# Optimization experiments

Measured on AMD Instinct MI355X. Metric: run time of the kernel, lower is better.

The kernel has to match this reference:

```python
import jax, jax.numpy as jnp
import numpy as np

B, P, C, O = 64, 24564, 81, 20
THRESHOLD = 0.5
NEG_POS_RATIO = 3
ALPHA = 1.0


def cxcy_to_xy(c):
    return jnp.concatenate([c[..., :2] - c[..., 2:] / 2, c[..., :2] + c[..., 2:] / 2], -1)


def xy_to_cxcy(x):
    return jnp.concatenate([(x[..., :2] + x[..., 2:]) / 2, x[..., 2:] - x[..., :2]], -1)


def cxcy_to_gcxgcy(c, p):
    # SSD box encoding with variances (10, 5)
    return jnp.concatenate([(c[..., :2] - p[..., :2]) / (p[..., 2:] / 10.0),
                            jnp.log(c[..., 2:] / p[..., 2:]) * 5.0], -1)


def jaccard(a, b):
    # a: [O,4] xy, b: [P,4] xy -> [O,P]
    lt = jnp.maximum(a[:, None, :2], b[None, :, :2])
    rb = jnp.minimum(a[:, None, 2:], b[None, :, 2:])
    wh = jnp.clip(rb - lt, 0.0)
    inter = wh[..., 0] * wh[..., 1]
    area_a = (a[:, 2] - a[:, 0]) * (a[:, 3] - a[:, 1])
    area_b = (b[:, 2] - b[:, 0]) * (b[:, 3] - b[:, 1])
    union = area_a[:, None] + area_b[None, :] - inter
    return inter / union


def smooth_l1(x):
    ax = jnp.abs(x)
    return jnp.where(ax < 1.0, 0.5 * ax * ax, ax - 0.5)


def setup_inputs() -> dict:
    key = jax.random.key(0)
    k1, k2, k3, k4, k5, k6, k7 = jax.random.split(key, 7)
    predicted_locs = jax.random.normal(k1, (B, P, 4), jnp.float32)
    predicted_scores = jax.random.normal(k2, (B, P, C), jnp.float32)
    # valid ground-truth boxes in boundary (xy) coords
    cxy = jax.random.uniform(k3, (B, O, 2), jnp.float32, 0.2, 0.8)
    wh = jax.random.uniform(k4, (B, O, 2), jnp.float32, 0.05, 0.3)
    boxes = jnp.concatenate([cxy - wh / 2, cxy + wh / 2], -1)
    labels = jax.random.randint(k5, (B, O), 1, C).astype(jnp.int64)
    pxy = jax.random.uniform(k6, (P, 2), jnp.float32, 0.0, 1.0)
    pwh = jax.random.uniform(k7, (P, 2), jnp.float32, 0.05, 0.5)
    priors_cxcy = jnp.concatenate([pxy, pwh], -1)
    return {"predicted_locs": predicted_locs, "predicted_scores": predicted_scores,
            "boxes": boxes, "labels": labels, "priors_cxcy": priors_cxcy}


def reference(predicted_locs, predicted_scores, boxes, labels, priors_cxcy):
    priors_xy = cxcy_to_xy(priors_cxcy)
    n_priors = priors_cxcy.shape[0]

    def match(boxes_i, labels_i):
        overlap = jaccard(boxes_i, priors_xy)                 # [O,P]
        overlap_fp = overlap.max(axis=0)                      # [P]
        object_fp = overlap.argmax(axis=0)                    # [P]
        prior_fo = overlap.argmax(axis=1)                     # [O]
        object_fp = object_fp.at[prior_fo].set(jnp.arange(O))
        overlap_fp = overlap_fp.at[prior_fo].set(1.0)
        label_fp = labels_i[object_fp]
        label_fp = jnp.where(overlap_fp < THRESHOLD, 0, label_fp)
        true_locs_i = cxcy_to_gcxgcy(xy_to_cxcy(boxes_i[object_fp]), priors_cxcy)
        return true_locs_i, label_fp

    true_locs, true_classes = jax.vmap(match)(boxes, labels)  # [B,P,4], [B,P]

    positive = true_classes != 0                              # [B,P]
    n_positives = positive.sum(axis=1)                        # [B]
    total_pos = n_positives.sum()

    # confidence loss per prior (categorical CE, no reduction)
    logp = jax.nn.log_softmax(predicted_scores, axis=-1)
    conf_loss_all = -jnp.take_along_axis(logp, true_classes[..., None], axis=-1)[..., 0]  # [B,P]

    # location loss: smooth L1, mean over positive box elements
    posf = positive.astype(predicted_locs.dtype)
    loc_elems = smooth_l1(predicted_locs - true_locs) * posf[..., None]
    loc_loss = jnp.sum(loc_elems) / jnp.maximum(4.0 * total_pos.astype(loc_elems.dtype), 1.0)

    # hard negative mining
    conf_loss_pos_sum = jnp.sum(conf_loss_all * posf)
    conf_loss_neg = jnp.where(positive, 0.0, conf_loss_all)
    conf_loss_neg = -jnp.sort(-conf_loss_neg, axis=1)         # descending per row
    n_hard_neg = NEG_POS_RATIO * n_positives
    hard_mask = jnp.arange(n_priors)[None, :] < n_hard_neg[:, None]
    conf_loss_hard_neg_sum = jnp.sum(conf_loss_neg * hard_mask.astype(conf_loss_neg.dtype))

    conf_loss_matched = (conf_loss_hard_neg_sum + conf_loss_pos_sum) / jnp.maximum(
        total_pos.astype(conf_loss_all.dtype), 1.0)

    loss = jnp.where(total_pos > 0,
                     conf_loss_matched + ALPHA * loc_loss,
                     jnp.mean(conf_loss_all))
    return loss
```

## Files before the change

kernel.cpp:

```cpp
#include <hip/hip_runtime.h>
#include <math.h>

#define B_ 64
#define P_ 24564
#define C_ 81
#define O_ 20

__device__ __forceinline__ float iou_xy(float ax0, float ay0, float ax1, float ay1,
                                        float bx0, float by0, float bx1, float by1) {
#pragma clang fp contract(off)
    float lx = fmaxf(ax0, bx0), ly = fmaxf(ay0, by0);
    float rx = fminf(ax1, bx1), ry = fminf(ay1, by1);
    float w = fmaxf(rx - lx, 0.f), h = fmaxf(ry - ly, 0.f);
    float inter = w * h;
    float aa = (ax1 - ax0) * (ay1 - ay0);
    float ab = (bx1 - bx0) * (by1 - by0);
    return inter / (aa + ab - inter);
}

__device__ __forceinline__ float sl1(float d) {
#pragma clang fp contract(off)
    float a = fabsf(d);
    return a < 1.f ? 0.5f * a * a : a - 0.5f;
}

__global__ void k_prior(const float* __restrict__ boxes, const float* __restrict__ priors,
                        int* __restrict__ prior_fo, int* __restrict__ n_pos,
                        float* __restrict__ pos_sum, float* __restrict__ tot_sum,
                        float* __restrict__ loc_sum) {
#pragma clang fp contract(off)
    int o = blockIdx.x, b = blockIdx.y, t = threadIdx.x;
    if (o == 0 && t == 0) {
        n_pos[b] = 0; pos_sum[b] = 0.f; tot_sum[b] = 0.f; loc_sum[b] = 0.f;
    }
    const float* bx = boxes + ((size_t)b * O_ + o) * 4;
    float bx0 = bx[0], by0 = bx[1], bx1 = bx[2], by1 = bx[3];
    float best = -1.f;
    int bi = 0;
    for (int p = t; p < P_; p += 256) {
        float4 pr = ((const float4*)priors)[p];
        float px0 = pr.x - pr.z * 0.5f, py0 = pr.y - pr.w * 0.5f;
        float px1 = pr.x + pr.z * 0.5f, py1 = pr.y + pr.w * 0.5f;
        float v = iou_xy(bx0, by0, bx1, by1, px0, py0, px1, py1);
        if (v > best) { best = v; bi = p; }
    }
    __shared__ float sv[256];
    __shared__ int si[256];
    sv[t] = best; si[t] = bi;
    __syncthreads();
    for (int s = 128; s > 0; s >>= 1) {
        if (t < s) {
            float ov = sv[t + s]; int oi = si[t + s];
            if (ov > sv[t] || (ov == sv[t] && oi < si[t])) { sv[t] = ov; si[t] = oi; }
        }
        __syncthreads();
    }
    if (t == 0) prior_fo[b * O_ + o] = si[0];
}

__global__ __launch_bounds__(256) void k_cm(const float* __restrict__ scores,
                                            const float* __restrict__ boxes,
                                            const int* __restrict__ labels,
                                            const float* __restrict__ priors,
                                            const float* __restrict__ plocs,
                                            const int* __restrict__ prior_fo,
                                            float* __restrict__ conf_neg,
                                            float* __restrict__ pos_sum,
                                            float* __restrict__ tot_sum,
                                            float* __restrict__ loc_sum,
                                            int* __restrict__ n_pos) {
#pragma clang fp contract(off)
    __shared__ float4 smem4[1296];
    float* smem = (float*)smem4;
    __shared__ float sb[O_][4];
    __shared__ float sc[O_][4];
    __shared__ int sl_[O_];
    __shared__ int sf[O_];
    int b = blockIdx.y;
    int p0 = blockIdx.x * 64;
    int t = threadIdx.x, lane = t & 63, w = t >> 6;
    int rows = P_ - p0;
    if (rows > 64) rows = 64;
    int nf4 = rows * 81 / 4;
    const float4* gsrc = (const float4*)(scores + ((size_t)b * P_ + p0) * (size_t)C_);
    for (int i = t; i < nf4; i += 256) smem4[i] = gsrc[i];
    if (t < O_) {
        const float* bx = boxes + ((size_t)b * O_ + t) * 4;
        float x0 = bx[0], y0 = bx[1], x1 = bx[2], y1 = bx[3];
        sb[t][0] = x0; sb[t][1] = y0; sb[t][2] = x1; sb[t][3] = y1;
        sc[t][0] = (x0 + x1) * 0.5f; sc[t][1] = (y0 + y1) * 0.5f;
        sc[t][2] = x1 - x0;          sc[t][3] = y1 - y0;
        sl_[t] = labels[b * O_ + t];
        sf[t] = prior_fo[b * O_ + t];
    }
    __syncthreads();

    int i = t >> 2;
    int q = t & 3;
    int p = p0 + i;
    bool active = (i < rows);

    int lab = 0;
    float lsum = 0.f;
    int posc = 0;
    if (active) {
        float4 pr = ((const float4*)priors)[p];
        float px0 = pr.x - pr.z * 0.5f, py0 = pr.y - pr.w * 0.5f;
        float px1 = pr.x + pr.z * 0.5f, py1 = pr.y + pr.w * 0.5f;
        float best = -1.f;
        int bi = 0x7fffffff;
        for (int o = q; o < O_; o += 4) {
            float v = iou_xy(sb[o][0], sb[o][1], sb[o][2], sb[o][3], px0, py0, px1, py1);
            if (v > best || (v == best && o < bi)) { best = v; bi = o; }
        }
#pragma unroll
        for (int off = 1; off <= 2; off <<= 1) {
            float ov = __shfl_xor(best, off);
            int oi = __shfl_xor(bi, off);
            if (ov > best || (ov == best && oi < bi)) { best = ov; bi = oi; }
        }
        for (int o = 0; o < O_; o++)
            if (sf[o] == p) { bi = o; best = 1.0f; }
        lab = (best < 0.5f) ? 0 : sl_[bi];
        if (lab != 0 && q == 0) {
            posc = 1;
            float gx = (sc[bi][0] - pr.x) / (pr.z / 10.0f);
            float gy = (sc[bi][1] - pr.y) / (pr.w / 10.0f);
            float gw = logf(sc[bi][2] / pr.z) * 5.0f;
            float gh = logf(sc[bi][3] / pr.w) * 5.0f;
            float4 pl = ((const float4*)plocs)[(size_t)b * P_ + p];
            lsum = sl1(pl.x - gx) + sl1(pl.y - gy) + sl1(pl.z - gw) + sl1(pl.w - gh);
        }
    }
    int tcv = lab;

    float sum = 0.f, st = 0.f;
    if (active) {
        int base = q * 21;
        int cnt = (q == 3) ? 18 : 21;
        const float* r = smem + i * 81 + base;
        for (int j = 0; j < cnt; j++) {
            float v = r[j];
            sum += __expf(v);
            if (base + j == tcv) st = v;
        }
    }
    sum += __shfl_xor(sum, 1);
    sum += __shfl_xor(sum, 2);
    st += __shfl_xor(st, 1);
    st += __shfl_xor(st, 2);

    float ce = 0.f, posv = 0.f;
    if (active) {
        ce = __logf(sum) - st;
        if (tcv != 0) posv = ce;
        if (q == 0) conf_neg[(size_t)b * P_ + p] = (tcv == 0) ? ce : 0.f;
    }
    float tc_ = (q == 0) ? ce : 0.f;
    float pc_ = (q == 0) ? posv : 0.f;
    for (int off = 32; off > 0; off >>= 1) {
        tc_ += __shfl_down(tc_, off);
        pc_ += __shfl_down(pc_, off);
        lsum += __shfl_down(lsum, off);
        posc += __shfl_down(posc, off);
    }
    __shared__ float stt[4], spp[4], sll[4];
    __shared__ int snn[4];
    if (lane == 0) { stt[w] = tc_; spp[w] = pc_; sll[w] = lsum; snn[w] = posc; }
    __syncthreads();
    if (t == 0) {
        atomicAdd(&tot_sum[b], stt[0] + stt[1] + stt[2] + stt[3]);
        atomicAdd(&pos_sum[b], spp[0] + spp[1] + spp[2] + spp[3]);
        int n4 = snn[0] + snn[1] + snn[2] + snn[3];
        if (n4 != 0) {
            atomicAdd(&loc_sum[b], sll[0] + sll[1] + sll[2] + sll[3]);
            atomicAdd(&n_pos[b], n4);
        }
    }
}

__global__ __launch_bounds__(1024) void k_topk(const float* __restrict__ conf_neg,
                                               const int* __restrict__ n_pos,
                                               float* __restrict__ hard_sum) {
    int b = blockIdx.x, t = threadIdx.x, lane = t & 63;
    const float* row = conf_neg + (size_t)b * P_;
    unsigned vb[24];
#pragma unroll
    for (int i = 0; i < 24; i++) {
        int p = t + (i << 10);
        vb[i] = (p < P_) ? __float_as_uint(row[p]) : 0u;
    }
    int k = 3 * n_pos[b];
    __shared__ int cnts[32];
    __shared__ float ssum;
    __shared__ int scnt;
    if (k <= 0) {
        if (t == 0) hard_sum[b] = 0.f;
        return;
    }
    if (t < 32) cnts[t] = 0;
    if (t == 0) { ssum = 0.f; scnt = 0; }
    __syncthreads();
    unsigned lo = 0u, hi = 0x7F800000u;
    int pass = 0;
    while (lo < hi) {
        unsigned mid = lo + ((hi - lo) >> 1);
        int c = 0;
#pragma unroll
        for (int i = 0; i < 24; i++) c += (vb[i] > mid);
        for (int off = 32; off > 0; off >>= 1) c += __shfl_down(c, off);
        if (lane == 0) atomicAdd(&cnts[pass], c);
        __syncthreads();
        int cnt = cnts[pass];
        if (cnt < k) hi = mid; else lo = mid + 1;
        pass++;
    }
    float s = 0.f;
    int c = 0;
#pragma unroll
    for (int i = 0; i < 24; i++) {
        if (vb[i] > lo) { s += __uint_as_float(vb[i]); c++; }
    }
    for (int off = 32; off > 0; off >>= 1) {
        s += __shfl_down(s, off);
        c += __shfl_down(c, off);
    }
    if (lane == 0) { atomicAdd(&ssum, s); atomicAdd(&scnt, c); }
    __syncthreads();
    if (t == 0) hard_sum[b] = ssum + (float)(k - scnt) * __uint_as_float(lo);
}

__global__ void k_final(const int* __restrict__ n_pos, const float* __restrict__ pos_sum,
                        const float* __restrict__ tot_sum, const float* __restrict__ loc_sum,
                        const float* __restrict__ hard_sum, float* __restrict__ out) {
    int t = threadIdx.x;
    int np = n_pos[t];
    float ps = pos_sum[t], ts = tot_sum[t], ls = loc_sum[t], hs = hard_sum[t];
    for (int off = 32; off > 0; off >>= 1) {
        np += __shfl_down(np, off);
        ps += __shfl_down(ps, off);
        ts += __shfl_down(ts, off);
        ls += __shfl_down(ls, off);
        hs += __shfl_down(hs, off);
    }
    if (t == 0) {
        float tp = (float)np;
        float conf = (hs + ps) / fmaxf(tp, 1.f);
        float loc = ls / fmaxf(4.f * tp, 1.f);
        float mean = ts / ((float)B_ * (float)P_);
        out[0] = (np > 0) ? (conf + loc) : mean;
    }
}

extern "C" void kernel_launch(void* const* d_in, const int* in_sizes, int n_in,
                              void* d_out, int out_size, void* d_ws, size_t ws_size,
                              hipStream_t stream) {
    const float* plocs  = (const float*)d_in[0];
    const float* scores = (const float*)d_in[1];
    const float* boxes  = (const float*)d_in[2];
    const int*   labels = (const int*)d_in[3];
    const float* priors = (const float*)d_in[4];

    char* ws = (char*)d_ws;
    float* conf_neg   = (float*)ws;
    int*   prior_fo   = (int*)(ws + (size_t)B_ * P_ * 4);
    int*   n_pos      = prior_fo + B_ * O_;
    float* pos_sum    = (float*)(n_pos + B_);
    float* tot_sum    = pos_sum + B_;
    float* loc_sum    = tot_sum + B_;
    float* hard_sum   = loc_sum + B_;

    k_prior<<<dim3(O_, B_), 256, 0, stream>>>(boxes, priors, prior_fo,
                                              n_pos, pos_sum, tot_sum, loc_sum);
    k_cm<<<dim3((P_ + 63) / 64, B_), 256, 0, stream>>>(
        scores, boxes, labels, priors, plocs, prior_fo,
        conf_neg, pos_sum, tot_sum, loc_sum, n_pos);
    k_topk<<<B_, 1024, 0, stream>>>(conf_neg, n_pos, hard_sum);
    k_final<<<1, 64, 0, stream>>>(n_pos, pos_sum, tot_sum, loc_sum, hard_sum, (float*)d_out);
}
```

Measured before the change: 861.3 us.

## Batch five boxes per block in prior matching and unroll score loads

```diff
diff --git a/kernel.cpp b/kernel.cpp
--- a/kernel.cpp
+++ b/kernel.cpp
@@ -24,38 +24,61 @@
     return a < 1.f ? 0.5f * a * a : a - 0.5f;
 }
 
-__global__ void k_prior(const float* __restrict__ boxes, const float* __restrict__ priors,
-                        int* __restrict__ prior_fo, int* __restrict__ n_pos,
-                        float* __restrict__ pos_sum, float* __restrict__ tot_sum,
-                        float* __restrict__ loc_sum) {
+__global__ __launch_bounds__(512) void k_prior(const float* __restrict__ boxes,
+                                               const float* __restrict__ priors,
+                                               int* __restrict__ prior_fo, int* __restrict__ n_pos,
+                                               float* __restrict__ pos_sum, float* __restrict__ tot_sum,
+                                               float* __restrict__ loc_sum) {
 #pragma clang fp contract(off)
-    int o = blockIdx.x, b = blockIdx.y, t = threadIdx.x;
-    if (o == 0 && t == 0) {
+    int g = blockIdx.x, b = blockIdx.y, t = threadIdx.x;
+    int lane = t & 63, w = t >> 6;
+    if (g == 0 && t == 0) {
         n_pos[b] = 0; pos_sum[b] = 0.f; tot_sum[b] = 0.f; loc_sum[b] = 0.f;
     }
-    const float* bx = boxes + ((size_t)b * O_ + o) * 4;
-    float bx0 = bx[0], by0 = bx[1], bx1 = bx[2], by1 = bx[3];
-    float best = -1.f;
-    int bi = 0;
-    for (int p = t; p < P_; p += 256) {
+    __shared__ float sbx[5][4];
+    if (t < 20) ((float*)sbx)[t] = boxes[((size_t)b * O_ + 5 * g) * 4 + t];
+    __syncthreads();
+
+    float bv[5];
+    int bi[5];
+#pragma unroll
+    for (int k = 0; k < 5; k++) { bv[k] = -1.f; bi[k] = 0; }
+
+    for (int p = t; p < P_; p += 512) {
         float4 pr = ((const float4*)priors)[p];
         float px0 = pr.x - pr.z * 0.5f, py0 = pr.y - pr.w * 0.5f;
         float px1 = pr.x + pr.z * 0.5f, py1 = pr.y + pr.w * 0.5f;
-        float v = iou_xy(bx0, by0, bx1, by1, px0, py0, px1, py1);
-        if (v > best) { best = v; bi = p; }
-    }
-    __shared__ float sv[256];
-    __shared__ int si[256];
-    sv[t] = best; si[t] = bi;
-    __syncthreads();
-    for (int s = 128; s > 0; s >>= 1) {
-        if (t < s) {
-            float ov = sv[t + s]; int oi = si[t + s];
-            if (ov > sv[t] || (ov == sv[t] && oi < si[t])) { sv[t] = ov; si[t] = oi; }
-        }
-        __syncthreads();
-    }
-    if (t == 0) prior_fo[b * O_ + o] = si[0];
+#pragma unroll
+        for (int k = 0; k < 5; k++) {
+            float v = iou_xy(sbx[k][0], sbx[k][1], sbx[k][2], sbx[k][3], px0, py0, px1, py1);
+            if (v > bv[k]) { bv[k] = v; bi[k] = p; }
+        }
+    }
+#pragma unroll
+    for (int k = 0; k < 5; k++) {
+        for (int off = 32; off > 0; off >>= 1) {
+            float ov = __shfl_down(bv[k], off);
+            int oi = __shfl_down(bi[k], off);
+            if (ov > bv[k] || (ov == bv[k] && oi < bi[k])) { bv[k] = ov; bi[k] = oi; }
+        }
+    }
+    __shared__ float swv[8][5];
+    __shared__ int swi[8][5];
+    if (lane == 0) {
+#pragma unroll
+        for (int k = 0; k < 5; k++) { swv[w][k] = bv[k]; swi[w][k] = bi[k]; }
+    }
+    __syncthreads();
+    if (t < 5) {
+        float best = swv[0][t];
+        int besti = swi[0][t];
+#pragma unroll
+        for (int ww = 1; ww < 8; ww++) {
+            float ov = swv[ww][t]; int oi = swi[ww][t];
+            if (ov > best || (ov == best && oi < besti)) { best = ov; besti = oi; }
+        }
+        prior_fo[b * O_ + 5 * g + t] = besti;
+    }
 }
 
 __global__ __launch_bounds__(256) void k_cm(const float* __restrict__ scores,
@@ -70,7 +93,7 @@
                                             float* __restrict__ loc_sum,
                                             int* __restrict__ n_pos) {
 #pragma clang fp contract(off)
-    __shared__ float4 smem4[1296];
+    __shared__ float4 smem4[1297];
     float* smem = (float*)smem4;
     __shared__ float sb[O_][4];
     __shared__ float sc[O_][4];
@@ -81,9 +104,15 @@
     int t = threadIdx.x, lane = t & 63, w = t >> 6;
     int rows = P_ - p0;
     if (rows > 64) rows = 64;
-    int nf4 = rows * 81 / 4;
     const float4* gsrc = (const float4*)(scores + ((size_t)b * P_ + p0) * (size_t)C_);
-    for (int i = t; i < nf4; i += 256) smem4[i] = gsrc[i];
+    if (rows == 64) {
+#pragma unroll
+        for (int u = 0; u < 5; u++) smem4[t + u * 256] = gsrc[t + u * 256];
+        if (t < 16) smem4[t + 1280] = gsrc[t + 1280];
+    } else {
+        int nf4 = rows * 81 / 4;
+        for (int i = t; i < nf4; i += 256) smem4[i] = gsrc[i];
+    }
     if (t < O_) {
         const float* bx = boxes + ((size_t)b * O_ + t) * 4;
         float x0 = bx[0], y0 = bx[1], x1 = bx[2], y1 = bx[3];
@@ -109,6 +138,7 @@
         float px1 = pr.x + pr.z * 0.5f, py1 = pr.y + pr.w * 0.5f;
         float best = -1.f;
         int bi = 0x7fffffff;
+#pragma unroll
         for (int o = q; o < O_; o += 4) {
             float v = iou_xy(sb[o][0], sb[o][1], sb[o][2], sb[o][3], px0, py0, px1, py1);
             if (v > best || (v == best && o < bi)) { best = v; bi = o; }
@@ -119,6 +149,7 @@
             int oi = __shfl_xor(bi, off);
             if (ov > best || (ov == best && oi < bi)) { best = ov; bi = oi; }
         }
+#pragma unroll
         for (int o = 0; o < O_; o++)
             if (sf[o] == p) { bi = o; best = 1.0f; }
         lab = (best < 0.5f) ? 0 : sl_[bi];
@@ -139,9 +170,11 @@
         int base = q * 21;
         int cnt = (q == 3) ? 18 : 21;
         const float* r = smem + i * 81 + base;
-        for (int j = 0; j < cnt; j++) {
+#pragma unroll
+        for (int j = 0; j < 21; j++) {
             float v = r[j];
-            sum += __expf(v);
+            float e = __expf(v);
+            sum += (j < cnt) ? e : 0.f;
             if (base + j == tcv) st = v;
         }
     }
@@ -270,8 +303,8 @@
     float* loc_sum    = tot_sum + B_;
     float* hard_sum   = loc_sum + B_;
 
-    k_prior<<<dim3(O_, B_), 256, 0, stream>>>(boxes, priors, prior_fo,
-                                              n_pos, pos_sum, tot_sum, loc_sum);
+    k_prior<<<dim3(4, B_), 512, 0, stream>>>(boxes, priors, prior_fo,
+                                             n_pos, pos_sum, tot_sum, loc_sum);
     k_cm<<<dim3((P_ + 63) / 64, B_), 256, 0, stream>>>(
         scores, boxes, labels, priors, plocs, prior_fo,
         conf_neg, pos_sum, tot_sum, loc_sum, n_pos);
```

After: 821.5 us. 1.05x faster.
